# Optimization experiments

Hardware: AMD Instinct MI355X
Metric: run time of the kernel (lower is better)

## Reference

```python
import jax, jax.numpy as jnp
import numpy as np

FEATURE_DIM = 256
NUM_HEADS = 8
HEAD_DIM = FEATURE_DIM // NUM_HEADS
LOCAL_RADIUS = 3.0
N_CUR = 4096
N_HIST = 4096
COORD_EXTENT = 16.0


def setup_inputs() -> dict:
    key = jax.random.key(0)
    ks = jax.random.split(key, 12)
    s = 1.0 / np.sqrt(FEATURE_DIM)  # ~nn.Linear init scale
    return {
        "current_feats": jax.random.normal(ks[0], (N_CUR, FEATURE_DIM), jnp.float32),
        "historical_feats": jax.random.normal(ks[1], (N_HIST, FEATURE_DIM), jnp.float32),
        "current_coords": jax.random.uniform(ks[2], (N_CUR, 3), jnp.float32) * COORD_EXTENT,
        "historical_coords": jax.random.uniform(ks[3], (N_HIST, 3), jnp.float32) * COORD_EXTENT,
        "Wq": jax.random.normal(ks[4], (FEATURE_DIM, FEATURE_DIM), jnp.float32) * s,
        "bq": jnp.zeros((FEATURE_DIM,), jnp.float32),
        "Wk": jax.random.normal(ks[5], (FEATURE_DIM, FEATURE_DIM), jnp.float32) * s,
        "bk": jnp.zeros((FEATURE_DIM,), jnp.float32),
        "Wv": jax.random.normal(ks[6], (FEATURE_DIM, FEATURE_DIM), jnp.float32) * s,
        "bv": jnp.zeros((FEATURE_DIM,), jnp.float32),
        "Wo": jax.random.normal(ks[7], (FEATURE_DIM, FEATURE_DIM), jnp.float32) * s,
        "bo": jnp.zeros((FEATURE_DIM,), jnp.float32),
    }


def reference(current_feats, historical_feats, current_coords, historical_coords,
              Wq, bq, Wk, bk, Wv, bv, Wo, bo):
    # local mask: squared distance <= radius^2 (identical to norm <= radius)
    diff = current_coords[:, None, :] - historical_coords[None, :, :]  # [Nq, Nk, 3]
    local_mask = jnp.sum(diff * diff, axis=-1) <= LOCAL_RADIUS ** 2      # [Nq, Nk]

    q = (current_feats @ Wq.T + bq).reshape(N_CUR, NUM_HEADS, HEAD_DIM)
    k = (historical_feats @ Wk.T + bk).reshape(N_HIST, NUM_HEADS, HEAD_DIM)
    v = (historical_feats @ Wv.T + bv).reshape(N_HIST, NUM_HEADS, HEAD_DIM)

    scores = jnp.einsum('qhd,khd->qhk', q, k) / np.sqrt(HEAD_DIM)        # [Nq, H, Nk]
    scores = jnp.where(local_mask[:, None, :], scores, -jnp.inf)
    attn = jax.nn.softmax(scores, axis=-1)  # dropout is identity in eval
    out = jnp.einsum('qhk,khd->qhd', attn, v).reshape(N_CUR, FEATURE_DIM)
    return out @ Wo.T + bo
```

## Files before the change

### kernel.cpp

```cpp
#include <hip/hip_runtime.h>
#include <math.h>

#define FDIM 256
#define NH 8
#define HD 32
#define NQ 4096
#define NKEY 4096
#define CAP 512
#define R2 9.0f

typedef _Float16 half8 __attribute__((ext_vector_type(8)));
typedef _Float16 half2v __attribute__((ext_vector_type(2)));
typedef float f32x4 __attribute__((ext_vector_type(4)));
typedef unsigned short ushort_t;

__device__ __forceinline__ void mfma_tile_16x64_f32AW(const float* __restrict__ A,
                                                      const float* __restrict__ W,
                                                      int m0, int n0, int wave, int lane,
                                                      f32x4 acc[4]) {
    const int row  = lane & 15;
    const int quad = lane >> 4;
    const float* aptr = A + (size_t)(m0 + wave * 16 + row) * 256 + quad * 8;
    const float* wptr = W + (size_t)(n0 + row) * 256 + quad * 8;
#pragma unroll
    for (int i = 0; i < 4; ++i) acc[i] = (f32x4){0.f, 0.f, 0.f, 0.f};
#pragma unroll
    for (int k0 = 0; k0 < 8; ++k0) {
        float4 a0 = *(const float4*)(aptr + k0 * 32);
        float4 a1 = *(const float4*)(aptr + k0 * 32 + 4);
        half8 a;
        a[0] = (_Float16)a0.x; a[1] = (_Float16)a0.y;
        a[2] = (_Float16)a0.z; a[3] = (_Float16)a0.w;
        a[4] = (_Float16)a1.x; a[5] = (_Float16)a1.y;
        a[6] = (_Float16)a1.z; a[7] = (_Float16)a1.w;
#pragma unroll
        for (int nt = 0; nt < 4; ++nt) {
            float4 b0 = *(const float4*)(wptr + (size_t)nt * 16 * 256 + k0 * 32);
            float4 b1 = *(const float4*)(wptr + (size_t)nt * 16 * 256 + k0 * 32 + 4);
            half8 b;
            b[0] = (_Float16)b0.x; b[1] = (_Float16)b0.y;
            b[2] = (_Float16)b0.z; b[3] = (_Float16)b0.w;
            b[4] = (_Float16)b1.x; b[5] = (_Float16)b1.y;
            b[6] = (_Float16)b1.z; b[7] = (_Float16)b1.w;
            acc[nt] = __builtin_amdgcn_mfma_f32_16x16x32_f16(a, b, acc[nt], 0, 0, 0);
        }
    }
}

__device__ __forceinline__ void mfma_tile_16x64_f16A_f32W(const _Float16* __restrict__ A,
                                                          const float* __restrict__ W,
                                                          int m0, int n0, int wave, int lane,
                                                          f32x4 acc[4]) {
    const int row  = lane & 15;
    const int quad = lane >> 4;
    const _Float16* aptr = A + (size_t)(m0 + wave * 16 + row) * 256 + quad * 8;
    const float* wptr = W + (size_t)(n0 + row) * 256 + quad * 8;
#pragma unroll
    for (int i = 0; i < 4; ++i) acc[i] = (f32x4){0.f, 0.f, 0.f, 0.f};
#pragma unroll
    for (int k0 = 0; k0 < 8; ++k0) {
        half8 a = *(const half8*)(aptr + k0 * 32);
#pragma unroll
        for (int nt = 0; nt < 4; ++nt) {
            float4 b0 = *(const float4*)(wptr + (size_t)nt * 16 * 256 + k0 * 32);
            float4 b1 = *(const float4*)(wptr + (size_t)nt * 16 * 256 + k0 * 32 + 4);
            half8 b;
            b[0] = (_Float16)b0.x; b[1] = (_Float16)b0.y;
            b[2] = (_Float16)b0.z; b[3] = (_Float16)b0.w;
            b[4] = (_Float16)b1.x; b[5] = (_Float16)b1.y;
            b[6] = (_Float16)b1.z; b[7] = (_Float16)b1.w;
            acc[nt] = __builtin_amdgcn_mfma_f32_16x16x32_f16(a, b, acc[nt], 0, 0, 0);
        }
    }
}

__global__ __launch_bounds__(256) void prep_qkv(const float* __restrict__ cur,
                                                const float* __restrict__ histf,
                                                const float* __restrict__ Wq,
                                                const float* __restrict__ Wk,
                                                const float* __restrict__ Wv,
                                                const float* __restrict__ qc,
                                                const float* __restrict__ kc,
                                                const float* __restrict__ bq,
                                                const float* __restrict__ bk,
                                                const float* __restrict__ bv,
                                                _Float16* __restrict__ Qh,
                                                _Float16* __restrict__ KV,
                                                ushort_t* __restrict__ nbr,
                                                int* __restrict__ cnt) {
    const int b    = blockIdx.x;
    const int wave = threadIdx.x >> 6;
    const int lane = threadIdx.x & 63;

    if (b < 768) {
        const int z   = b >> 8;
        const int rem = b & 255;
        const int m0  = (rem >> 2) * 64;
        const int n0  = (rem & 3) * 64;

        const float* A    = (z == 0) ? cur : histf;
        const float* W    = (z == 0) ? Wq : (z == 1) ? Wk : Wv;
        const float* bias = (z == 0) ? bq : (z == 1) ? bk : bv;

        f32x4 acc[4];
        mfma_tile_16x64_f32AW(A, W, m0, n0, wave, lane, acc);

        const int col  = lane & 15;
        const int quad = lane >> 4;
        float bs[4];
#pragma unroll
        for (int nt = 0; nt < 4; ++nt) bs[nt] = bias[n0 + nt * 16 + col];

        if (z == 0) {
#pragma unroll
            for (int nt = 0; nt < 4; ++nt)
#pragma unroll
                for (int r = 0; r < 4; ++r)
                    Qh[(size_t)(m0 + wave * 16 + quad * 4 + r) * 256 +
                       n0 + nt * 16 + col] = (_Float16)(acc[nt][r] + bs[nt]);
        } else {
            const int off = (z == 1) ? 0 : 256;
#pragma unroll
            for (int nt = 0; nt < 4; ++nt)
#pragma unroll
                for (int r = 0; r < 4; ++r)
                    KV[(size_t)(m0 + wave * 16 + quad * 4 + r) * 512 + off +
                       n0 + nt * 16 + col] = (_Float16)(acc[nt][r] + bs[nt]);
        }
    } else {
        const int q  = (b - 768) * 4 + wave;
        const float qx = qc[q * 3 + 0];
        const float qy = qc[q * 3 + 1];
        const float qz = qc[q * 3 + 2];
        int base = 0;
        for (int k0 = 0; k0 < NKEY; k0 += 64) {
            const int k = k0 + lane;
            float dx = __fsub_rn(qx, kc[k * 3 + 0]);
            float dy = __fsub_rn(qy, kc[k * 3 + 1]);
            float dz = __fsub_rn(qz, kc[k * 3 + 2]);
            float d2 = __fadd_rn(__fadd_rn(__fmul_rn(dx, dx), __fmul_rn(dy, dy)),
                                 __fmul_rn(dz, dz));
            bool valid = (d2 <= R2);
            unsigned long long bal = __ballot(valid);
            if (valid) {
                int pos = base + __popcll(bal & ((1ull << lane) - 1ull));
                if (pos < CAP) nbr[(size_t)q * CAP + pos] = (ushort_t)k;
            }
            base += __popcll(bal);
        }
        if (lane == 0) cnt[q] = (base > CAP) ? CAP : base;
    }
}

__global__ __launch_bounds__(256) void sparse_attn11(const _Float16* __restrict__ Qh,
                                                     const _Float16* __restrict__ KV,
                                                     const ushort_t* __restrict__ nbr,
                                                     const int* __restrict__ cnt,
                                                     _Float16* __restrict__ Ob) {
    __shared__ float sm[4][32][12];
    const int q    = blockIdx.x;
    const int t    = threadIdx.x;
    const int wave = t >> 6;
    const int lane = t & 63;
    const int p    = lane >> 5;
    const int h    = (lane >> 2) & 7;
    const int s    = lane & 3;
    const int koff = h * HD + s * 8;
    const float sc = 0.17677669529663687f;

    const half8 qh = *(const half8*)(Qh + (size_t)q * FDIM + koff);

    float o[8];
#pragma unroll
    for (int i = 0; i < 8; ++i) o[i] = 0.f;
    float l = 0.f;

    const int n = cnt[q];
    const ushort_t* nl = nbr + (size_t)q * CAP;

    for (int j = 2 * wave + p; j < n; j += 8) {
        const int k = nl[j];
        const _Float16* r = KV + ((size_t)k << 9) + koff;
        half8 k8 = *(const half8*)(r);
        half8 v8 = *(const half8*)(r + 256);

        float part = 0.f;
#pragma unroll
        for (int i = 0; i < 4; ++i) {
            half2v qa, ka;
            qa[0] = qh[2 * i]; qa[1] = qh[2 * i + 1];
            ka[0] = k8[2 * i]; ka[1] = k8[2 * i + 1];
#if defined(__has_builtin) && __has_builtin(__builtin_amdgcn_fdot2)
            part = __builtin_amdgcn_fdot2(qa, ka, part, false);
#else
            part = fmaf((float)qa[0], (float)ka[0], part);
            part = fmaf((float)qa[1], (float)ka[1], part);
#endif
        }
        part += __shfl_xor(part, 1, 64);
        part += __shfl_xor(part, 2, 64);

        const float pw = __expf(part * sc);
        l += pw;
#pragma unroll
        for (int i = 0; i < 8; ++i)
            o[i] = fmaf(pw, (float)v8[i], o[i]);
    }

    l += __shfl_xor(l, 32, 64);
#pragma unroll
    for (int i = 0; i < 8; ++i) o[i] += __shfl_xor(o[i], 32, 64);

    if (lane < 32) {
        float* dst = &sm[wave][lane][0];
        *(float4*)(dst)     = (float4){o[0], o[1], o[2], o[3]};
        *(float4*)(dst + 4) = (float4){o[4], o[5], o[6], o[7]};
        dst[8] = l;
    }
    __syncthreads();

    if (t < 32) {
        float4 x0 = *(const float4*)&sm[0][t][0];
        float4 x1 = *(const float4*)&sm[0][t][4];
        float O[8] = {x0.x, x0.y, x0.z, x0.w, x1.x, x1.y, x1.z, x1.w};
        float L = sm[0][t][8];
#pragma unroll
        for (int w = 1; w < 4; ++w) {
            float4 y0 = *(const float4*)&sm[w][t][0];
            float4 y1 = *(const float4*)&sm[w][t][4];
            L += sm[w][t][8];
            O[0] += y0.x; O[1] += y0.y; O[2] += y0.z; O[3] += y0.w;
            O[4] += y1.x; O[5] += y1.y; O[6] += y1.z; O[7] += y1.w;
        }
        const float inv = 1.0f / L;
        half8 ho;
#pragma unroll
        for (int i = 0; i < 8; ++i) ho[i] = (_Float16)(O[i] * inv);
        *(half8*)(Ob + (size_t)q * FDIM + t * 8) = ho;
    }
}

__global__ __launch_bounds__(256) void o_mfma(const _Float16* __restrict__ Ob,
                                              const float* __restrict__ Wo,
                                              const float* __restrict__ bo,
                                              float* __restrict__ out) {
    const int wave = threadIdx.x >> 6;
    const int lane = threadIdx.x & 63;
    const int m0   = blockIdx.y * 64;
    const int n0   = blockIdx.x * 64;

    f32x4 acc[4];
    mfma_tile_16x64_f16A_f32W(Ob, Wo, m0, n0, wave, lane, acc);

    const int col  = lane & 15;
    const int quad = lane >> 4;
#pragma unroll
    for (int nt = 0; nt < 4; ++nt) {
        const float b = bo[n0 + nt * 16 + col];
#pragma unroll
        for (int r = 0; r < 4; ++r)
            out[(size_t)(m0 + wave * 16 + quad * 4 + r) * 256 + n0 + nt * 16 + col] =
                acc[nt][r] + b;
    }
}

extern "C" void kernel_launch(void* const* d_in, const int* in_sizes, int n_in,
                              void* d_out, int out_size, void* d_ws, size_t ws_size,
                              hipStream_t stream) {
    const float* cur_feats   = (const float*)d_in[0];
    const float* hist_feats  = (const float*)d_in[1];
    const float* cur_coords  = (const float*)d_in[2];
    const float* hist_coords = (const float*)d_in[3];
    const float* Wq = (const float*)d_in[4];
    const float* bq = (const float*)d_in[5];
    const float* Wk = (const float*)d_in[6];
    const float* bk = (const float*)d_in[7];
    const float* Wv = (const float*)d_in[8];
    const float* bv = (const float*)d_in[9];
    const float* Wo = (const float*)d_in[10];
    const float* bo = (const float*)d_in[11];
    float* out = (float*)d_out;

    char* w = (char*)d_ws;
    _Float16*  Qh  = (_Float16*)(w);
    _Float16*  KV  = (_Float16*)(w + (4 << 20));
    ushort_t*  nbr = (ushort_t*)(w + (8 << 20));
    int*       cnt = (int*)(w + (12 << 20));
    _Float16*  Ob  = (_Float16*)(w + (12 << 20) + (64 << 10));

    prep_qkv<<<1792, 256, 0, stream>>>(cur_feats, hist_feats, Wq, Wk, Wv,
                                       cur_coords, hist_coords, bq, bk, bv,
                                       Qh, KV, nbr, cnt);

    sparse_attn11<<<NQ, 256, 0, stream>>>(Qh, KV, nbr, cnt, Ob);

    o_mfma<<<dim3(4, 64), 256, 0, stream>>>(Ob, Wo, bo, out);
}
```

Baseline: 159.1 us.

## Split neighbor search into key halves and interleave GEMM with search blocks

The neighbor-list build now gives each query two waves, each scanning half the keys into its own 256-slot sub-list with a separate count. Block indices interleave 3 GEMM tiles with 8 search blocks per group of 11, so the GEMM and search work mix across the grid instead of running in two phases. The attention kernel walks both sub-lists. It pre-scales Q to fp32 once and uses plain fp32 FMAs instead of fdot2. This shortens the serial search chain per wave and balances load, at the cost of a per-half cap that could truncate dense halves differently from the old single cap.

```diff
diff --git a/kernel.cpp b/kernel.cpp
--- a/kernel.cpp
+++ b/kernel.cpp
@@ -7,10 +7,10 @@
 #define NQ 4096
 #define NKEY 4096
 #define CAP 512
+#define HCAP 256
 #define R2 9.0f
 
 typedef _Float16 half8 __attribute__((ext_vector_type(8)));
-typedef _Float16 half2v __attribute__((ext_vector_type(2)));
 typedef float f32x4 __attribute__((ext_vector_type(4)));
 typedef unsigned short ushort_t;
 
@@ -89,12 +89,15 @@
                                                 ushort_t* __restrict__ nbr,
                                                 int* __restrict__ cnt) {
     const int b    = blockIdx.x;
+    const int g    = b / 11;
+    const int r    = b % 11;
     const int wave = threadIdx.x >> 6;
     const int lane = threadIdx.x & 63;
 
-    if (b < 768) {
-        const int z   = b >> 8;
-        const int rem = b & 255;
+    if (r < 3) {
+        const int id  = g * 3 + r;
+        const int z   = id >> 8;
+        const int rem = id & 255;
         const int m0  = (rem >> 2) * 64;
         const int n0  = (rem & 3) * 64;
 
@@ -115,25 +118,29 @@
 #pragma unroll
             for (int nt = 0; nt < 4; ++nt)
 #pragma unroll
-                for (int r = 0; r < 4; ++r)
-                    Qh[(size_t)(m0 + wave * 16 + quad * 4 + r) * 256 +
-                       n0 + nt * 16 + col] = (_Float16)(acc[nt][r] + bs[nt]);
+                for (int rr = 0; rr < 4; ++rr)
+                    Qh[(size_t)(m0 + wave * 16 + quad * 4 + rr) * 256 +
+                       n0 + nt * 16 + col] = (_Float16)(acc[nt][rr] + bs[nt]);
         } else {
             const int off = (z == 1) ? 0 : 256;
 #pragma unroll
             for (int nt = 0; nt < 4; ++nt)
 #pragma unroll
-                for (int r = 0; r < 4; ++r)
-                    KV[(size_t)(m0 + wave * 16 + quad * 4 + r) * 512 + off +
-                       n0 + nt * 16 + col] = (_Float16)(acc[nt][r] + bs[nt]);
+                for (int rr = 0; rr < 4; ++rr)
+                    KV[(size_t)(m0 + wave * 16 + quad * 4 + rr) * 512 + off +
+                       n0 + nt * 16 + col] = (_Float16)(acc[nt][rr] + bs[nt]);
         }
     } else {
-        const int q  = (b - 768) * 4 + wave;
+        const int idx  = g * 8 + (r - 3);
+        const int q    = idx * 2 + (wave >> 1);
+        const int half = wave & 1;
         const float qx = qc[q * 3 + 0];
         const float qy = qc[q * 3 + 1];
         const float qz = qc[q * 3 + 2];
+        ushort_t* dst = nbr + (size_t)q * CAP + half * HCAP;
         int base = 0;
-        for (int k0 = 0; k0 < NKEY; k0 += 64) {
+        const int k_lo = half * 2048;
+        for (int k0 = k_lo; k0 < k_lo + 2048; k0 += 64) {
             const int k = k0 + lane;
             float dx = __fsub_rn(qx, kc[k * 3 + 0]);
             float dy = __fsub_rn(qy, kc[k * 3 + 1]);
@@ -144,15 +151,15 @@
             unsigned long long bal = __ballot(valid);
             if (valid) {
                 int pos = base + __popcll(bal & ((1ull << lane) - 1ull));
-                if (pos < CAP) nbr[(size_t)q * CAP + pos] = (ushort_t)k;
+                if (pos < HCAP) dst[pos] = (ushort_t)k;
             }
             base += __popcll(bal);
         }
-        if (lane == 0) cnt[q] = (base > CAP) ? CAP : base;
-    }
-}
-
-__global__ __launch_bounds__(256) void sparse_attn11(const _Float16* __restrict__ Qh,
+        if (lane == 0) cnt[2 * q + half] = (base > HCAP) ? HCAP : base;
+    }
+}
+
+__global__ __launch_bounds__(256) void sparse_attn12(const _Float16* __restrict__ Qh,
                                                      const _Float16* __restrict__ KV,
                                                      const ushort_t* __restrict__ nbr,
                                                      const int* __restrict__ cnt,
@@ -166,45 +173,47 @@
     const int h    = (lane >> 2) & 7;
     const int s    = lane & 3;
     const int koff = h * HD + s * 8;
-    const float sc = 0.17677669529663687f;
-
-    const half8 qh = *(const half8*)(Qh + (size_t)q * FDIM + koff);
+
+    float qv[8];
+    {
+        half8 qh = *(const half8*)(Qh + (size_t)q * FDIM + koff);
+        const float sc = 0.17677669529663687f;
+#pragma unroll
+        for (int i = 0; i < 8; ++i) qv[i] = (float)qh[i] * sc;
+    }
 
     float o[8];
 #pragma unroll
     for (int i = 0; i < 8; ++i) o[i] = 0.f;
     float l = 0.f;
 
-    const int n = cnt[q];
+    const int c0 = cnt[2 * q];
+    const int c1 = cnt[2 * q + 1];
     const ushort_t* nl = nbr + (size_t)q * CAP;
 
-    for (int j = 2 * wave + p; j < n; j += 8) {
-        const int k = nl[j];
-        const _Float16* r = KV + ((size_t)k << 9) + koff;
-        half8 k8 = *(const half8*)(r);
-        half8 v8 = *(const half8*)(r + 256);
-
-        float part = 0.f;
-#pragma unroll
-        for (int i = 0; i < 4; ++i) {
-            half2v qa, ka;
-            qa[0] = qh[2 * i]; qa[1] = qh[2 * i + 1];
-            ka[0] = k8[2 * i]; ka[1] = k8[2 * i + 1];
-#if defined(__has_builtin) && __has_builtin(__builtin_amdgcn_fdot2)
-            part = __builtin_amdgcn_fdot2(qa, ka, part, false);
-#else
-            part = fmaf((float)qa[0], (float)ka[0], part);
-            part = fmaf((float)qa[1], (float)ka[1], part);
-#endif
-        }
-        part += __shfl_xor(part, 1, 64);
-        part += __shfl_xor(part, 2, 64);
-
-        const float pw = __expf(part * sc);
-        l += pw;
-#pragma unroll
-        for (int i = 0; i < 8; ++i)
-            o[i] = fmaf(pw, (float)v8[i], o[i]);
+#pragma unroll
+    for (int sub = 0; sub < 2; ++sub) {
+        const int n_s = sub ? c1 : c0;
+        const ushort_t* nls = nl + sub * HCAP;
+        for (int j = 2 * wave + p; j < n_s; j += 8) {
+            const int k = nls[j];
+            const _Float16* rr = KV + ((size_t)k << 9) + koff;
+            half8 k8 = *(const half8*)(rr);
+            half8 v8 = *(const half8*)(rr + 256);
+
+            float part = 0.f;
+#pragma unroll
+            for (int i = 0; i < 8; ++i)
+                part = fmaf(qv[i], (float)k8[i], part);
+            part += __shfl_xor(part, 1, 64);
+            part += __shfl_xor(part, 2, 64);
+
+            const float pw = __expf(part);
+            l += pw;
+#pragma unroll
+            for (int i = 0; i < 8; ++i)
+                o[i] = fmaf(pw, (float)v8[i], o[i]);
+        }
     }
 
     l += __shfl_xor(l, 32, 64);
@@ -288,11 +297,11 @@
     int*       cnt = (int*)(w + (12 << 20));
     _Float16*  Ob  = (_Float16*)(w + (12 << 20) + (64 << 10));
 
-    prep_qkv<<<1792, 256, 0, stream>>>(cur_feats, hist_feats, Wq, Wk, Wv,
+    prep_qkv<<<2816, 256, 0, stream>>>(cur_feats, hist_feats, Wq, Wk, Wv,
                                        cur_coords, hist_coords, bq, bk, bv,
                                        Qh, KV, nbr, cnt);
 
-    sparse_attn11<<<NQ, 256, 0, stream>>>(Qh, KV, nbr, cnt, Ob);
+    sparse_attn12<<<NQ, 256, 0, stream>>>(Qh, KV, nbr, cnt, Ob);
 
     o_mfma<<<dim3(4, 64), 256, 0, stream>>>(Ob, Wo, bo, out);
 }
```

Measured after the change: 169.3 us. 6.4% more time.
